# Kernel optimization log

Hardware: AMD Instinct MI355X
Metric: run time of the kernel (lower is better)

The kernel has to match this reference:

```python
import jax, jax.numpy as jnp
import numpy as np

HIDDEN = 2048
N_HEADS = 32
N_KV_HEADS = 8
HEAD_DIM = HIDDEN // N_HEADS  # 64
N_GROUPS = N_HEADS // N_KV_HEADS  # 4
EPS = 1e-6
BATCH = 2
SEQ = 2048


def setup_inputs() -> dict:
    key = jax.random.key(0)
    ks = jax.random.split(key, 8)
    s = 1.0 / np.sqrt(HIDDEN)
    return {
        "hidden_states": jax.random.normal(ks[0], (BATCH, SEQ, HIDDEN), jnp.float32),
        # torch nn.Linear weights: [out_features, in_features]
        "Wq": jax.random.normal(ks[1], (N_HEADS * HEAD_DIM, HIDDEN), jnp.float32) * s,
        "Wk": jax.random.normal(ks[2], (N_KV_HEADS * HEAD_DIM, HIDDEN), jnp.float32) * s,
        "Wv": jax.random.normal(ks[3], (N_KV_HEADS * HEAD_DIM, HIDDEN), jnp.float32) * s,
        "Wo": jax.random.normal(ks[4], (HIDDEN, N_HEADS * HEAD_DIM), jnp.float32) * s,
        "q_norm_weight": jnp.ones((HEAD_DIM,), jnp.float32),
        "k_norm_weight": jnp.ones((HEAD_DIM,), jnp.float32),
    }


def _rmsnorm(x, w, eps=EPS):
    # x: [..., head_dim]
    rms = jax.lax.rsqrt(jnp.mean(x * x, axis=-1, keepdims=True) + eps)
    return x * rms * w


def reference(hidden_states, Wq, Wk, Wv, Wo, q_norm_weight, k_norm_weight):
    B, S, _ = hidden_states.shape
    # projections (y = x @ W.T)
    q = jnp.einsum('bsh,oh->bso', hidden_states, Wq)
    k = jnp.einsum('bsh,oh->bso', hidden_states, Wk)
    v = jnp.einsum('bsh,oh->bso', hidden_states, Wv)
    # [B, H, S, D]
    q = q.reshape(B, S, N_HEADS, HEAD_DIM).transpose(0, 2, 1, 3)
    k = k.reshape(B, S, N_KV_HEADS, HEAD_DIM).transpose(0, 2, 1, 3)
    v = v.reshape(B, S, N_KV_HEADS, HEAD_DIM).transpose(0, 2, 1, 3)
    # GQA repeat_interleave along head dim
    k = jnp.repeat(k, N_GROUPS, axis=1)
    v = jnp.repeat(v, N_GROUPS, axis=1)
    # fused QK RMSNorm
    q = _rmsnorm(q, q_norm_weight)
    k = _rmsnorm(k, k_norm_weight)
    # scaled dot-product attention with causal mask
    scale = 1.0 / np.sqrt(HEAD_DIM)
    scores = jnp.einsum('bhqd,bhkd->bhqk', q, k) * scale
    causal = jnp.tril(jnp.ones((S, S), dtype=bool))
    scores = jnp.where(causal, scores, jnp.finfo(scores.dtype).min)
    attn = jax.nn.softmax(scores, axis=-1)
    out = jnp.einsum('bhqk,bhkd->bhqd', attn, v)  # [B, H, S, D]
    out = out.transpose(0, 2, 1, 3).reshape(B, S, N_HEADS * HEAD_DIM)
    return jnp.einsum('bso,ho->bsh', out, Wo)
```

## Files before the change

### kernel.cpp

```cpp
#include <hip/hip_runtime.h>

typedef _Float16 f16;
typedef _Float16 f16x8 __attribute__((ext_vector_type(8)));
typedef _Float16 f16x4 __attribute__((ext_vector_type(4)));
typedef float f32x4 __attribute__((ext_vector_type(4)));

#define HID 2048
#define NH 32
#define NKV 8
#define HD 64
#define SEQ 2048
#define NB 2

__device__ __forceinline__ void gload_lds16(const void* g, void* l) {
  __builtin_amdgcn_global_load_lds((const __attribute__((address_space(1))) void*)g,
                                   (__attribute__((address_space(3))) void*)l, 16, 0, 0);
}

__device__ __forceinline__ uint cvt_pk_f16(float a, float b) {
  auto v = __builtin_amdgcn_cvt_pkrtz(a, b);
  uint u;
  __builtin_memcpy(&u, &v, 4);
  return u;
}

__global__ __launch_bounds__(256) void cvt_all(const float* __restrict__ X,
                                               const float* __restrict__ Wq,
                                               const float* __restrict__ Wk,
                                               const float* __restrict__ Wv,
                                               const float* __restrict__ Wo,
                                               f16* __restrict__ Xb, f16* __restrict__ Wqb,
                                               f16* __restrict__ Wkb, f16* __restrict__ Wvb,
                                               f16* __restrict__ Wob) {
  long i = (long)blockIdx.x * 256 + threadIdx.x;
  const float* s; f16* d; long o;
  if (i < 2097152)      { s = X;  d = Xb;  o = i; }
  else if (i < 3145728) { s = Wq; d = Wqb; o = i - 2097152; }
  else if (i < 3407872) { s = Wk; d = Wkb; o = i - 3145728; }
  else if (i < 3670016) { s = Wv; d = Wvb; o = i - 3407872; }
  else                  { s = Wo; d = Wob; o = i - 3670016; }
  float4 v = ((const float4*)s)[o];
  f16x4 ov = { (f16)v.x, (f16)v.y, (f16)v.z, (f16)v.w };
  ((f16x4*)d)[o] = ov;
}

template <typename CT>
__global__ __launch_bounds__(256) void gemm_bt(const f16* __restrict__ A,
                                               const f16* __restrict__ Bm,
                                               CT* __restrict__ C0, CT* __restrict__ C1,
                                               int M, int N, int K,
                                               int n_split, int ldc0, int ldc1) {
  __shared__ f16 As[2][128 * 64];
  __shared__ f16 Bs[2][128 * 64];
  const int t = threadIdx.x;
  const int lane = t & 63;
  const int w = t >> 6;
  const int wr = w >> 1, wc = w & 1;
  const int g = lane >> 4;
  const int lr = lane & 15;

  const int nwg = gridDim.x * gridDim.y;
  const int orig = blockIdx.y * gridDim.x + blockIdx.x;
  const int wg = (orig & 7) * (nwg >> 3) + (orig >> 3);
  const int m0 = (wg / gridDim.x) * 128;
  const int n0 = (wg % gridDim.x) * 128;

  f32x4 acc[4][4] = {};

  const int nkt = K / 64;

  auto stage = [&](int buf, int kt) {
    const int k0 = kt * 64;
#pragma unroll
    for (int i = 0; i < 4; ++i) {
      int c = w * 4 + i;
      int o = c * 1024 + lane * 16;
      int row = o >> 7;
      int ss = ((o >> 4) & 7) ^ (row & 7);
      const char* srcA = (const char*)A + ((size_t)(m0 + row) * K + k0) * 2 + ss * 16;
      gload_lds16(srcA, (char*)(&As[buf][0]) + c * 1024);
      const char* srcB = (const char*)Bm + ((size_t)(n0 + row) * K + k0) * 2 + ss * 16;
      gload_lds16(srcB, (char*)(&Bs[buf][0]) + c * 1024);
    }
  };

  stage(0, 0);
  if (nkt > 1) stage(1, 1);
  for (int kt = 0; kt < nkt; ++kt) {
    const int cur = kt & 1;
    if (kt + 1 < nkt) asm volatile("s_waitcnt vmcnt(8)" ::: "memory");
    else              asm volatile("s_waitcnt vmcnt(0)" ::: "memory");
    __builtin_amdgcn_s_barrier();
    __builtin_amdgcn_sched_barrier(0);

    f16x8 af[2][4], bf[2][4];
#pragma unroll
    for (int ks = 0; ks < 2; ++ks)
#pragma unroll
      for (int mf = 0; mf < 4; ++mf) {
        int row = wr * 64 + mf * 16 + lr;
        int slot = (g + 4 * ks) ^ (row & 7);
        af[ks][mf] = *(const f16x8*)((const char*)(&As[cur][0]) + row * 128 + slot * 16);
      }
#pragma unroll
    for (int ks = 0; ks < 2; ++ks)
#pragma unroll
      for (int nf = 0; nf < 4; ++nf) {
        int row = wc * 64 + nf * 16 + lr;
        int slot = (g + 4 * ks) ^ (row & 7);
        bf[ks][nf] = *(const f16x8*)((const char*)(&Bs[cur][0]) + row * 128 + slot * 16);
      }
    asm volatile("s_waitcnt lgkmcnt(0)" ::: "memory");
    __builtin_amdgcn_sched_barrier(0);
    __builtin_amdgcn_s_barrier();

    if (kt + 2 < nkt) stage(cur, kt + 2);

    __builtin_amdgcn_s_setprio(1);
#pragma unroll
    for (int ks = 0; ks < 2; ++ks)
#pragma unroll
      for (int mf = 0; mf < 4; ++mf)
#pragma unroll
        for (int nf = 0; nf < 4; ++nf)
          acc[mf][nf] = __builtin_amdgcn_mfma_f32_16x16x32_f16(af[ks][mf], bf[ks][nf], acc[mf][nf], 0, 0, 0);
    __builtin_amdgcn_s_setprio(0);
  }

  CT* Cp; int ldc, nb;
  if (n0 < n_split) { Cp = C0; ldc = ldc0; nb = n0; }
  else              { Cp = C1; ldc = ldc1; nb = n0 - n_split; }
#pragma unroll
  for (int mf = 0; mf < 4; ++mf)
#pragma unroll
    for (int nf = 0; nf < 4; ++nf)
#pragma unroll
      for (int r = 0; r < 4; ++r) {
        int mm = m0 + wr * 64 + mf * 16 + g * 4 + r;
        int nn = nb + wc * 64 + nf * 16 + lr;
        Cp[(size_t)mm * ldc + nn] = (CT)acc[mf][nf][r];
      }
}

__global__ __launch_bounds__(256) void vtrans(f16* __restrict__ KV,
                                              f16* __restrict__ VT,
                                              const float* __restrict__ kw) {
  __shared__ f16 tile[64][72];
  int t = threadIdx.x;
  int st = blockIdx.x, hk = blockIdx.y, b = blockIdx.z;

#pragma unroll
  for (int p = 0; p < 2; ++p) {
    int idx = p * 256 + t;
    int s = idx >> 3, c8 = (idx & 7) * 8;
    f16* kp = KV + (size_t)(b * SEQ + st * 64 + s) * 1024 + hk * 64 + c8;
    f16x8 kv = *(const f16x8*)kp;
    float ss = 0.f;
#pragma unroll
    for (int j = 0; j < 8; ++j) { float x = (float)kv[j]; ss += x * x; }
    ss += __shfl_xor(ss, 1); ss += __shfl_xor(ss, 2); ss += __shfl_xor(ss, 4);
    float sc = rsqrtf(ss * (1.0f / 64.0f) + 1e-6f);
    f16x8 on;
#pragma unroll
    for (int j = 0; j < 8; ++j) on[j] = (f16)((float)kv[j] * sc * kw[c8 + j]);
    *(f16x8*)kp = on;
  }

#pragma unroll
  for (int p = 0; p < 2; ++p) {
    int idx = p * 256 + t;
    int s = idx >> 3, c8 = (idx & 7) * 8;
    f16x8 v = *(const f16x8*)(KV + (size_t)(b * SEQ + st * 64 + s) * 1024 + 512 + hk * 64 + c8);
    *(f16x8*)(&tile[s][c8]) = v;
  }
  __syncthreads();
#pragma unroll
  for (int p = 0; p < 2; ++p) {
    int idx = p * 256 + t;
    int d = idx >> 3, s8 = (idx & 7) * 8;
    f16x8 ov;
#pragma unroll
    for (int j = 0; j < 8; ++j) {
      int pos = s8 + j;
      int k = (pos & 32) | (((pos >> 2) & 1) << 4) | (((pos >> 4) & 1) << 3)
            | (((pos >> 3) & 1) << 2) | (pos & 3);
      ov[j] = tile[k][d];
    }
    *(f16x8*)(VT + ((size_t)((b * NKV + hk) * 64) + d) * SEQ + st * 64 + s8) = ov;
  }
}

__global__ __launch_bounds__(512) void attn(const f16* __restrict__ Q,
                                            const f16* __restrict__ KV,
                                            const f16* __restrict__ VT,
                                            f16* __restrict__ AO,
                                            const float* __restrict__ qw) {
  __shared__ f16 Ks[3][64 * 64];
  __shared__ f16 Vs[3][64 * 64];
  const int t = threadIdx.x, lane = t & 63, w = t >> 6;
  const int g = lane >> 4, lr = lane & 15;
  const int col = blockIdx.x;
  const int qt = 31 - blockIdx.y;
  const int b = col & 1;
  const int h = 2 * (col >> 1) + (w >> 2);
  const int rg = w & 3;
  const int hk = h >> 2;
  const int q0 = qt * 64;

  const size_t qrow = (size_t)(b * SEQ + q0 + rg * 16 + lr);
  f16x8 qf[2];
  qf[0] = *(const f16x8*)(Q + qrow * HID + h * 64 + g * 8);
  qf[1] = *(const f16x8*)(Q + qrow * HID + h * 64 + g * 8 + 32);

  {
    float ss = 0.f;
#pragma unroll
    for (int i = 0; i < 2; ++i)
#pragma unroll
      for (int j = 0; j < 8; ++j) { float x = (float)qf[i][j]; ss += x * x; }
    ss += __shfl_xor(ss, 16); ss += __shfl_xor(ss, 32);
    float sc = rsqrtf(ss * (1.0f / 64.0f) + 1e-6f) * (0.125f * 1.44269504f);
    const float4* qw4 = (const float4*)qw;
    float4 w0 = qw4[2 * g], w1 = qw4[2 * g + 1];
    float4 w2 = qw4[2 * g + 8], w3 = qw4[2 * g + 9];
    qf[0][0] = (f16)((float)qf[0][0] * sc * w0.x);
    qf[0][1] = (f16)((float)qf[0][1] * sc * w0.y);
    qf[0][2] = (f16)((float)qf[0][2] * sc * w0.z);
    qf[0][3] = (f16)((float)qf[0][3] * sc * w0.w);
    qf[0][4] = (f16)((float)qf[0][4] * sc * w1.x);
    qf[0][5] = (f16)((float)qf[0][5] * sc * w1.y);
    qf[0][6] = (f16)((float)qf[0][6] * sc * w1.z);
    qf[0][7] = (f16)((float)qf[0][7] * sc * w1.w);
    qf[1][0] = (f16)((float)qf[1][0] * sc * w2.x);
    qf[1][1] = (f16)((float)qf[1][1] * sc * w2.y);
    qf[1][2] = (f16)((float)qf[1][2] * sc * w2.z);
    qf[1][3] = (f16)((float)qf[1][3] * sc * w2.w);
    qf[1][4] = (f16)((float)qf[1][4] * sc * w3.x);
    qf[1][5] = (f16)((float)qf[1][5] * sc * w3.y);
    qf[1][6] = (f16)((float)qf[1][6] * sc * w3.z);
    qf[1][7] = (f16)((float)qf[1][7] * sc * w3.w);
  }

  int koff[2][4], voff[2][4];
#pragma unroll
  for (int ks = 0; ks < 2; ++ks)
#pragma unroll
    for (int nf = 0; nf < 4; ++nf) {
      int row = nf * 16 + lr;
      koff[ks][nf] = row * 128 + (((g + 4 * ks) ^ (row & 7)) * 16);
    }
#pragma unroll
  for (int m = 0; m < 2; ++m)
#pragma unroll
    for (int df = 0; df < 4; ++df) {
      int row = df * 16 + lr;
      voff[m][df] = row * 128 + (((4 * m + g) ^ (row & 7)) * 16);
    }

  f16x8 vones = { (f16)1.0f, (f16)1.0f, (f16)1.0f, (f16)1.0f,
                  (f16)1.0f, (f16)1.0f, (f16)1.0f, (f16)1.0f };

  f32x4 oacc[4] = {};
  f32x4 psacc = {};

  const int nkt = qt + 1;

  auto stage = [&](int buf, int kt2) {
    int o = w * 1024 + lane * 16;
    int row = o >> 7;
    int ss = ((o >> 4) & 7) ^ (row & 7);
    gload_lds16((const char*)KV + ((size_t)(b * SEQ + kt2 * 64 + row) * 1024 + hk * 64) * 2 + ss * 16,
                (char*)(&Ks[buf][0]) + w * 1024);
    gload_lds16((const char*)VT + (((size_t)((b * NKV + hk) * 64) + row) * SEQ + kt2 * 64) * 2 + ss * 16,
                (char*)(&Vs[buf][0]) + w * 1024);
  };

  stage(0, 0);
  if (nkt > 1) stage(1, 1);
  int cur = 0;
  for (int kt = 0; kt < nkt; ++kt) {
    if (kt + 1 < nkt) asm volatile("s_waitcnt vmcnt(2)" ::: "memory");
    else              asm volatile("s_waitcnt vmcnt(0)" ::: "memory");
    __builtin_amdgcn_s_barrier();
    asm volatile("" ::: "memory");

    if (kt + 2 < nkt) {
      int nb = cur + 2; if (nb >= 3) nb -= 3;
      stage(nb, kt + 2);
    }

    const char* Kb = (const char*)(&Ks[cur][0]);
    const char* Vb = (const char*)(&Vs[cur][0]);

    f32x4 sacc[4] = {};
#pragma unroll
    for (int ks = 0; ks < 2; ++ks) {
      __builtin_amdgcn_s_setprio(1);
#pragma unroll
      for (int nf = 0; nf < 4; ++nf) {
        f16x8 kf = *(const f16x8*)(Kb + koff[ks][nf]);
        sacc[nf] = __builtin_amdgcn_mfma_f32_16x16x32_f16(kf, qf[ks], sacc[nf], 0, 0, 0);
      }
      __builtin_amdgcn_s_setprio(0);
    }

    if (kt == qt) {
      int qq = q0 + rg * 16 + lr;
#pragma unroll
      for (int nf = 0; nf < 4; ++nf) {
        int kvb = kt * 64 + nf * 16 + g * 4;
#pragma unroll
        for (int r = 0; r < 4; ++r)
          if (kvb + r > qq) sacc[nf][r] = -1e30f;
      }
    }

    uint pk[8];
#pragma unroll
    for (int nf = 0; nf < 4; ++nf) {
      float p0 = exp2f(sacc[nf][0]);
      float p1 = exp2f(sacc[nf][1]);
      float p2 = exp2f(sacc[nf][2]);
      float p3 = exp2f(sacc[nf][3]);
      pk[2 * nf]     = cvt_pk_f16(p0, p1);
      pk[2 * nf + 1] = cvt_pk_f16(p2, p3);
    }

#pragma unroll
    for (int m = 0; m < 2; ++m) {
      union { uint u[4]; f16x8 v; } pu;
      pu.u[0] = pk[4 * m];     pu.u[1] = pk[4 * m + 1];
      pu.u[2] = pk[4 * m + 2]; pu.u[3] = pk[4 * m + 3];
      __builtin_amdgcn_s_setprio(1);
#pragma unroll
      for (int df = 0; df < 4; ++df) {
        f16x8 vf = *(const f16x8*)(Vb + voff[m][df]);
        oacc[df] = __builtin_amdgcn_mfma_f32_16x16x32_f16(pu.v, vf, oacc[df], 0, 0, 0);
      }
      psacc = __builtin_amdgcn_mfma_f32_16x16x32_f16(pu.v, vones, psacc, 0, 0, 0);
      __builtin_amdgcn_s_setprio(0);
    }

    cur = (cur == 2) ? 0 : cur + 1;
  }

  float pdiv[4];
#pragma unroll
  for (int r = 0; r < 4; ++r) pdiv[r] = 1.0f / psacc[r];

#pragma unroll
  for (int df = 0; df < 4; ++df)
#pragma unroll
    for (int r = 0; r < 4; ++r) {
      size_t rowg = (size_t)(b * SEQ + q0 + rg * 16 + g * 4 + r);
      AO[rowg * HID + h * 64 + df * 16 + lr] = (f16)(oacc[df][r] * pdiv[r]);
    }
}

extern "C" void kernel_launch(void* const* d_in, const int* in_sizes, int n_in,
                              void* d_out, int out_size, void* d_ws, size_t ws_size,
                              hipStream_t stream) {
  const float* X  = (const float*)d_in[0];
  const float* Wq = (const float*)d_in[1];
  const float* Wk = (const float*)d_in[2];
  const float* Wv = (const float*)d_in[3];
  const float* Wo = (const float*)d_in[4];
  const float* qw = (const float*)d_in[5];
  const float* kw = (const float*)d_in[6];

  char* ws = (char*)d_ws;
  f16* Xb   = (f16*)(ws + 0);
  f16* Wqkv = (f16*)(ws + 16777216);
  f16* Wob  = (f16*)(ws + 29360128);
  f16* Qb   = (f16*)(ws + 37748736);
  f16* KVb  = (f16*)(ws + 54525952);
  f16* VTb  = (f16*)(ws + 62914560);
  f16* AOb  = (f16*)(ws + 67108864);
  float* OUT = (float*)d_out;

  cvt_all<<<18432, 256, 0, stream>>>(X, Wq, Wk, Wv, Wo,
                                     Xb, Wqkv, Wqkv + 2048 * 2048, Wqkv + 2560 * 2048, Wob);

  gemm_bt<f16><<<dim3(24, 32), 256, 0, stream>>>(Xb, Wqkv, Qb, KVb,
                                                 4096, 3072, 2048, 2048, 2048, 1024);

  vtrans<<<dim3(32, 8, 2), 256, 0, stream>>>(KVb, VTb, kw);
  attn<<<dim3(32, 32, 1), 512, 0, stream>>>(Qb, KVb, VTb, AOb, qw);

  gemm_bt<float><<<dim3(16, 32), 256, 0, stream>>>(AOb, Wob, OUT, OUT,
                                                   4096, 2048, 2048, 2048, 2048, 2048);
}
```

Baseline: 177.0 us.

## Load K/V tiles directly from global memory instead of LDS triple buffering

Removes the shared-memory triple-buffered staging of K and V tiles, including the async global-to-LDS loads, waitcnt and barriers. Each wave now loads its K and V MFMA fragments straight from global memory (relying on L1/L2) at the start of each key tile. This drops LDS usage and block-wide synchronisation, which may raise occupancy. In exchange there is no prefetch overlap, global loads are strided (1024- or SEQ-element row stride), and the 8 waves of a block redundantly fetch the same K/V data.

```diff
diff --git a/kernel.cpp b/kernel.cpp
--- a/kernel.cpp
+++ b/kernel.cpp
@@ -195,8 +195,6 @@
                                             const f16* __restrict__ VT,
                                             f16* __restrict__ AO,
                                             const float* __restrict__ qw) {
-  __shared__ f16 Ks[3][64 * 64];
-  __shared__ f16 Vs[3][64 * 64];
   const int t = threadIdx.x, lane = t & 63, w = t >> 6;
   const int g = lane >> 4, lr = lane & 15;
   const int col = blockIdx.x;
@@ -241,22 +239,6 @@
     qf[1][7] = (f16)((float)qf[1][7] * sc * w3.w);
   }
 
-  int koff[2][4], voff[2][4];
-#pragma unroll
-  for (int ks = 0; ks < 2; ++ks)
-#pragma unroll
-    for (int nf = 0; nf < 4; ++nf) {
-      int row = nf * 16 + lr;
-      koff[ks][nf] = row * 128 + (((g + 4 * ks) ^ (row & 7)) * 16);
-    }
-#pragma unroll
-  for (int m = 0; m < 2; ++m)
-#pragma unroll
-    for (int df = 0; df < 4; ++df) {
-      int row = df * 16 + lr;
-      voff[m][df] = row * 128 + (((4 * m + g) ^ (row & 7)) * 16);
-    }
-
   f16x8 vones = { (f16)1.0f, (f16)1.0f, (f16)1.0f, (f16)1.0f,
                   (f16)1.0f, (f16)1.0f, (f16)1.0f, (f16)1.0f };
 
@@ -265,42 +247,33 @@
 
   const int nkt = qt + 1;
 
-  auto stage = [&](int buf, int kt2) {
-    int o = w * 1024 + lane * 16;
-    int row = o >> 7;
-    int ss = ((o >> 4) & 7) ^ (row & 7);
-    gload_lds16((const char*)KV + ((size_t)(b * SEQ + kt2 * 64 + row) * 1024 + hk * 64) * 2 + ss * 16,
-                (char*)(&Ks[buf][0]) + w * 1024);
-    gload_lds16((const char*)VT + (((size_t)((b * NKV + hk) * 64) + row) * SEQ + kt2 * 64) * 2 + ss * 16,
-                (char*)(&Vs[buf][0]) + w * 1024);
-  };
-
-  stage(0, 0);
-  if (nkt > 1) stage(1, 1);
-  int cur = 0;
+  const f16* Kb = KV + (size_t)b * SEQ * 1024 + hk * 64;
+  const f16* Vb = VT + ((size_t)(b * NKV + hk) * 64) * SEQ;
+
   for (int kt = 0; kt < nkt; ++kt) {
-    if (kt + 1 < nkt) asm volatile("s_waitcnt vmcnt(2)" ::: "memory");
-    else              asm volatile("s_waitcnt vmcnt(0)" ::: "memory");
-    __builtin_amdgcn_s_barrier();
-    asm volatile("" ::: "memory");
-
-    if (kt + 2 < nkt) {
-      int nb = cur + 2; if (nb >= 3) nb -= 3;
-      stage(nb, kt + 2);
-    }
-
-    const char* Kb = (const char*)(&Ks[cur][0]);
-    const char* Vb = (const char*)(&Vs[cur][0]);
+    const f16* Kt = Kb + (size_t)kt * 64 * 1024;
+    const f16* Vt = Vb + kt * 64;
+
+    f16x8 kf[2][4];
+#pragma unroll
+    for (int ks = 0; ks < 2; ++ks)
+#pragma unroll
+      for (int nf = 0; nf < 4; ++nf)
+        kf[ks][nf] = *(const f16x8*)(Kt + (size_t)(nf * 16 + lr) * 1024 + (g + 4 * ks) * 8);
+    f16x8 vf[2][4];
+#pragma unroll
+    for (int m = 0; m < 2; ++m)
+#pragma unroll
+      for (int df = 0; df < 4; ++df)
+        vf[m][df] = *(const f16x8*)(Vt + (size_t)(df * 16 + lr) * SEQ + (4 * m + g) * 8);
 
     f32x4 sacc[4] = {};
 #pragma unroll
     for (int ks = 0; ks < 2; ++ks) {
       __builtin_amdgcn_s_setprio(1);
 #pragma unroll
-      for (int nf = 0; nf < 4; ++nf) {
-        f16x8 kf = *(const f16x8*)(Kb + koff[ks][nf]);
-        sacc[nf] = __builtin_amdgcn_mfma_f32_16x16x32_f16(kf, qf[ks], sacc[nf], 0, 0, 0);
-      }
+      for (int nf = 0; nf < 4; ++nf)
+        sacc[nf] = __builtin_amdgcn_mfma_f32_16x16x32_f16(kf[ks][nf], qf[ks], sacc[nf], 0, 0, 0);
       __builtin_amdgcn_s_setprio(0);
     }
 
@@ -333,15 +306,11 @@
       pu.u[2] = pk[4 * m + 2]; pu.u[3] = pk[4 * m + 3];
       __builtin_amdgcn_s_setprio(1);
 #pragma unroll
-      for (int df = 0; df < 4; ++df) {
-        f16x8 vf = *(const f16x8*)(Vb + voff[m][df]);
-        oacc[df] = __builtin_amdgcn_mfma_f32_16x16x32_f16(pu.v, vf, oacc[df], 0, 0, 0);
-      }
+      for (int df = 0; df < 4; ++df)
+        oacc[df] = __builtin_amdgcn_mfma_f32_16x16x32_f16(pu.v, vf[m][df], oacc[df], 0, 0, 0);
       psacc = __builtin_amdgcn_mfma_f32_16x16x32_f16(pu.v, vones, psacc, 0, 0, 0);
       __builtin_amdgcn_s_setprio(0);
     }
-
-    cur = (cur == 2) ? 0 : cur + 1;
   }
 
   float pdiv[4];
```

New measurement: 355.3 us. 101% more time.

## Use 128-wide KV tiles with double-buffered LDS staging in attention

Applied to the files above, without the earlier changes.

Doubles the KV tile from 64 to 128 keys per iteration and replaces the triple-buffer ring with a double buffer, adding a trailing barrier before refilling the just-consumed buffer. Each iteration now does twice the MFMA work per barrier and stage call, which cuts loop and synchronization overhead. In exchange there is an extra barrier per iteration, less prefetch depth, and more causal-masking waste on the diagonal tile when the query tile index is even (half the last tile is masked). LDS usage grows from 48KB to 64KB per block.

```diff
diff --git a/kernel.cpp b/kernel.cpp
--- a/kernel.cpp
+++ b/kernel.cpp
@@ -195,8 +195,8 @@
                                             const f16* __restrict__ VT,
                                             f16* __restrict__ AO,
                                             const float* __restrict__ qw) {
-  __shared__ f16 Ks[3][64 * 64];
-  __shared__ f16 Vs[3][64 * 64];
+  __shared__ f16 Ks[2][128 * 64];
+  __shared__ f16 Vs[2][64 * 128];
   const int t = threadIdx.x, lane = t & 63, w = t >> 6;
   const int g = lane >> 4, lr = lane & 15;
   const int col = blockIdx.x;
@@ -241,20 +241,20 @@
     qf[1][7] = (f16)((float)qf[1][7] * sc * w3.w);
   }
 
-  int koff[2][4], voff[2][4];
+  int koff[2][8], voff[4][4];
 #pragma unroll
   for (int ks = 0; ks < 2; ++ks)
 #pragma unroll
-    for (int nf = 0; nf < 4; ++nf) {
+    for (int nf = 0; nf < 8; ++nf) {
       int row = nf * 16 + lr;
       koff[ks][nf] = row * 128 + (((g + 4 * ks) ^ (row & 7)) * 16);
     }
 #pragma unroll
-  for (int m = 0; m < 2; ++m)
+  for (int m = 0; m < 4; ++m)
 #pragma unroll
     for (int df = 0; df < 4; ++df) {
       int row = df * 16 + lr;
-      voff[m][df] = row * 128 + (((4 * m + g) ^ (row & 7)) * 16);
+      voff[m][df] = row * 256 + (((4 * m + g) ^ (row & 7)) * 16);
     }
 
   f16x8 vones = { (f16)1.0f, (f16)1.0f, (f16)1.0f, (f16)1.0f,
@@ -263,61 +263,62 @@
   f32x4 oacc[4] = {};
   f32x4 psacc = {};
 
-  const int nkt = qt + 1;
+  const int nkt = (qt + 2) >> 1;
 
   auto stage = [&](int buf, int kt2) {
-    int o = w * 1024 + lane * 16;
-    int row = o >> 7;
-    int ss = ((o >> 4) & 7) ^ (row & 7);
-    gload_lds16((const char*)KV + ((size_t)(b * SEQ + kt2 * 64 + row) * 1024 + hk * 64) * 2 + ss * 16,
-                (char*)(&Ks[buf][0]) + w * 1024);
-    gload_lds16((const char*)VT + (((size_t)((b * NKV + hk) * 64) + row) * SEQ + kt2 * 64) * 2 + ss * 16,
-                (char*)(&Vs[buf][0]) + w * 1024);
+#pragma unroll
+    for (int i = 0; i < 2; ++i) {
+      int c = w * 2 + i;
+      int o = c * 1024 + lane * 16;
+      int krow = o >> 7;
+      int kss = ((o >> 4) & 7) ^ (krow & 7);
+      gload_lds16((const char*)KV + ((size_t)(b * SEQ + kt2 * 128 + krow) * 1024 + hk * 64) * 2 + kss * 16,
+                  (char*)(&Ks[buf][0]) + c * 1024);
+      int vrow = o >> 8;
+      int vss = ((o >> 4) & 15) ^ (vrow & 7);
+      gload_lds16((const char*)VT + (((size_t)((b * NKV + hk) * 64) + vrow) * SEQ + kt2 * 128) * 2 + vss * 16,
+                  (char*)(&Vs[buf][0]) + c * 1024);
+    }
   };
 
   stage(0, 0);
   if (nkt > 1) stage(1, 1);
-  int cur = 0;
   for (int kt = 0; kt < nkt; ++kt) {
-    if (kt + 1 < nkt) asm volatile("s_waitcnt vmcnt(2)" ::: "memory");
+    const int cur = kt & 1;
+    if (kt + 1 < nkt) asm volatile("s_waitcnt vmcnt(4)" ::: "memory");
     else              asm volatile("s_waitcnt vmcnt(0)" ::: "memory");
     __builtin_amdgcn_s_barrier();
-    asm volatile("" ::: "memory");
-
-    if (kt + 2 < nkt) {
-      int nb = cur + 2; if (nb >= 3) nb -= 3;
-      stage(nb, kt + 2);
-    }
+    __builtin_amdgcn_sched_barrier(0);
 
     const char* Kb = (const char*)(&Ks[cur][0]);
     const char* Vb = (const char*)(&Vs[cur][0]);
 
-    f32x4 sacc[4] = {};
+    f32x4 sacc[8] = {};
 #pragma unroll
     for (int ks = 0; ks < 2; ++ks) {
       __builtin_amdgcn_s_setprio(1);
 #pragma unroll
-      for (int nf = 0; nf < 4; ++nf) {
+      for (int nf = 0; nf < 8; ++nf) {
         f16x8 kf = *(const f16x8*)(Kb + koff[ks][nf]);
         sacc[nf] = __builtin_amdgcn_mfma_f32_16x16x32_f16(kf, qf[ks], sacc[nf], 0, 0, 0);
       }
       __builtin_amdgcn_s_setprio(0);
     }
 
-    if (kt == qt) {
+    if (kt == nkt - 1) {
       int qq = q0 + rg * 16 + lr;
 #pragma unroll
-      for (int nf = 0; nf < 4; ++nf) {
-        int kvb = kt * 64 + nf * 16 + g * 4;
+      for (int nf = 0; nf < 8; ++nf) {
+        int kvb = kt * 128 + nf * 16 + g * 4;
 #pragma unroll
         for (int r = 0; r < 4; ++r)
           if (kvb + r > qq) sacc[nf][r] = -1e30f;
       }
     }
 
-    uint pk[8];
-#pragma unroll
-    for (int nf = 0; nf < 4; ++nf) {
+    uint pk[16];
+#pragma unroll
+    for (int nf = 0; nf < 8; ++nf) {
       float p0 = exp2f(sacc[nf][0]);
       float p1 = exp2f(sacc[nf][1]);
       float p2 = exp2f(sacc[nf][2]);
@@ -327,7 +328,7 @@
     }
 
 #pragma unroll
-    for (int m = 0; m < 2; ++m) {
+    for (int m = 0; m < 4; ++m) {
       union { uint u[4]; f16x8 v; } pu;
       pu.u[0] = pk[4 * m];     pu.u[1] = pk[4 * m + 1];
       pu.u[2] = pk[4 * m + 2]; pu.u[3] = pk[4 * m + 3];
@@ -341,7 +342,10 @@
       __builtin_amdgcn_s_setprio(0);
     }
 
-    cur = (cur == 2) ? 0 : cur + 1;
+    asm volatile("s_waitcnt lgkmcnt(0)" ::: "memory");
+    __builtin_amdgcn_sched_barrier(0);
+    __builtin_amdgcn_s_barrier();
+    if (kt + 2 < nkt) stage(cur, kt + 2);
   }
 
   float pdiv[4];
```

Measured after the change: 181.1 us. 2.3% more time.
